# Performance work log

Measured on AMD Instinct MI355X. Metric: run time of the kernel, lower is better.

## Reference

```python
import jax, jax.numpy as jnp
import numpy as np


def grid_sample_bilinear(img, grid):
    """Replicates torch F.grid_sample(mode='bilinear', padding_mode='zeros',
    align_corners=False). img: [B,C,Hin,Win]; grid: [B,Ho,Wo,2] in [-1,1]
    with grid[...,0]=x (width), grid[...,1]=y (height). Returns [B,C,Ho,Wo]."""
    B, C, Hin, Win = img.shape
    x = (grid[..., 0] + 1.0) * (Win * 0.5) - 0.5  # unnormalized pixel coords
    y = (grid[..., 1] + 1.0) * (Hin * 0.5) - 0.5
    x0 = jnp.floor(x)
    y0 = jnp.floor(y)
    wx1 = x - x0
    wy1 = y - y0

    def tap(xi, yi, w):
        valid = ((xi >= 0) & (xi < Win) & (yi >= 0) & (yi < Hin)).astype(img.dtype)
        xc = jnp.clip(xi, 0, Win - 1).astype(jnp.int32)
        yc = jnp.clip(yi, 0, Hin - 1).astype(jnp.int32)
        def gather_one(im, yb, xb, wb):
            return im[:, yb, xb] * wb[None]  # [C,Ho,Wo]
        return jax.vmap(gather_one)(img, yc, xc, valid * w)

    return (tap(x0, y0, (1.0 - wx1) * (1.0 - wy1))
            + tap(x0 + 1.0, y0, wx1 * (1.0 - wy1))
            + tap(x0, y0 + 1.0, (1.0 - wx1) * wy1)
            + tap(x0 + 1.0, y0 + 1.0, wx1 * wy1))


def setup_inputs() -> dict:
    key = jax.random.key(0)
    k_uv, k1, k2, k3, k4 = jax.random.split(key, 5)
    W, H = 2048, 2048
    B, Ho, Wo = 8, 1024, 1024
    return {
        "uv": jax.random.uniform(k_uv, (B, Ho, Wo, 2), dtype=jnp.float32),
        "layer1": jax.random.normal(k1, (1, 1, W, H), dtype=jnp.float32),
        "layer2": jax.random.normal(k2, (1, 1, W // 2, H // 2), dtype=jnp.float32),
        "layer3": jax.random.normal(k3, (1, 1, W // 4, H // 4), dtype=jnp.float32),
        "layer4": jax.random.normal(k4, (1, 1, W // 8, H // 8), dtype=jnp.float32),
    }


def reference(uv, layer1, layer2, layer3, layer4):
    B = uv.shape[0]
    grid = uv * 2.0 - 1.0
    y = None
    for layer in (layer1, layer2, layer3, layer4):
        img = jnp.broadcast_to(layer, (B,) + layer.shape[1:])  # repeat(B,1,1,1)
        s = grid_sample_bilinear(img, grid)
        y = s if y is None else y + s
    return y  # [B,1,Ho,Wo]
```

## Files before the change

### kernel.cpp

```cpp
#include <hip/hip_runtime.h>
#include <hip/hip_fp16.h>


typedef unsigned int u32x2 __attribute__((ext_vector_type(2)));
typedef unsigned int u32x4 __attribute__((ext_vector_type(4)));
typedef float f32x4 __attribute__((ext_vector_type(4)));

#define K 1024
#define CHUNK 4096
#define HB 4096
#define SEG (CHUNK * 256)
#define NXCD 8

__device__ __forceinline__ int binof(float u, float v) {
    int bx = min(max((int)(u * 32.0f), 0), 31);
    int by = min(max((int)(v * 32.0f), 0), 31);
    return by * 32 + bx;
}

__global__ __launch_bounds__(256) void repack_hist_kernel(
    const float* __restrict__ l1, const float* __restrict__ l2,
    const float* __restrict__ l3, const float* __restrict__ l4,
    __half2* __restrict__ r1, __half2* __restrict__ r2,
    __half2* __restrict__ r3, __half2* __restrict__ r4,
    const float2* __restrict__ uv, unsigned* __restrict__ hist, int n) {
    const int n1 = 2048 * 2048, n2 = 1024 * 1024, n3 = 512 * 512, n4 = 256 * 256;
    int i = blockIdx.x * 256 + threadIdx.x;
    {
        const float* __restrict__ src = nullptr;
        __half2* __restrict__ dst = nullptr;
        int S = 0, logS = 0, j = 0;
        if (i < n1) {
            src = l1; dst = r1; S = 2048; logS = 11; j = i;
        } else if (i < n1 + n2) {
            src = l2; dst = r2; S = 1024; logS = 10; j = i - n1;
        } else if (i < n1 + n2 + n3) {
            src = l3; dst = r3; S = 512; logS = 9; j = i - (n1 + n2);
        } else if (i < n1 + n2 + n3 + n4) {
            src = l4; dst = r4; S = 256; logS = 8; j = i - (n1 + n2 + n3);
        }
        if (src) {
            int y = j >> logS;
            float a = src[j];
            float b = src[(y < S - 1) ? (j + S) : j];
            dst[j] = __halves2half2(__float2half(a), __float2half(b));
        }
    }
    if (hist == nullptr) return;
    int base = blockIdx.x * HB;
    if (base >= n) return;
    __shared__ unsigned cnt[K];
    for (int b = threadIdx.x; b < K; b += 256) cnt[b] = 0u;
    __syncthreads();
    int m = min(HB, n - base);
    const f32x4* uv4 = (const f32x4*)(uv + base);
    int npair = m >> 1;
    for (int k2 = threadIdx.x; k2 < npair; k2 += 256) {
        f32x4 q = __builtin_nontemporal_load(&uv4[k2]);
        atomicAdd(&cnt[binof(q.x, q.y)], 1u);
        atomicAdd(&cnt[binof(q.z, q.w)], 1u);
    }
    if ((m & 1) && threadIdx.x == 0) {
        float2 q = uv[base + m - 1];
        atomicAdd(&cnt[binof(q.x, q.y)], 1u);
    }
    __syncthreads();
    int seg = base / SEG;
    unsigned* gh = hist + (size_t)seg * K;
    for (int b = threadIdx.x; b < K; b += 256) {
        unsigned v = cnt[b];
        if (v) atomicAdd(&gh[b], v);
    }
}

__global__ __launch_bounds__(256) void scan_kernel(
    const unsigned* __restrict__ hist, unsigned* __restrict__ cursor) {
    int seg = blockIdx.x;
    const unsigned* h = hist + (size_t)seg * K;
    unsigned* c = cursor + (size_t)seg * K;
    __shared__ unsigned part[256];
    int t = threadIdx.x;
    unsigned v0 = h[t * 4], v1 = h[t * 4 + 1], v2 = h[t * 4 + 2], v3 = h[t * 4 + 3];
    unsigned s1 = v0, s2 = v0 + v1, s3 = v0 + v1 + v2;
    part[t] = s3 + v3;
    __syncthreads();
    for (int off = 1; off < 256; off <<= 1) {
        unsigned x = (t >= off) ? part[t - off] : 0u;
        __syncthreads();
        part[t] += x;
        __syncthreads();
    }
    unsigned tb = (t > 0) ? part[t - 1] : 0u;
    unsigned segstart = (unsigned)((size_t)seg * SEG);
    c[t * 4] = segstart + tb;
    c[t * 4 + 1] = segstart + tb + s1;
    c[t * 4 + 2] = segstart + tb + s2;
    c[t * 4 + 3] = segstart + tb + s3;
}

__global__ __launch_bounds__(256) void partition_kernel(
    const float2* __restrict__ uv, unsigned* __restrict__ cursor,
    float2* __restrict__ uv_s, unsigned* __restrict__ invp, int n, int pinned) {
    __shared__ float2 ssort[CHUNK];
    __shared__ unsigned cnt[K];
    __shared__ unsigned lbase[K];
    __shared__ unsigned gdiff[K];
    __shared__ unsigned part[256];
    int t = threadIdx.x;
    int blk = blockIdx.x;
    int c = pinned ? ((blk % NXCD) * (SEG / CHUNK) + blk / NXCD) : blk;
    int cb = c * CHUNK;
    if (cb >= n) return;
    int cnum = min(CHUNK, n - cb);
    int seg = cb / SEG;

    for (int b = t; b < K; b += 256) cnt[b] = 0u;
    __syncthreads();
    const f32x4* uv4 = (const f32x4*)(uv + cb);
    int npair = cnum >> 1;
    for (int k2 = t; k2 < npair; k2 += 256) {
        f32x4 q = uv4[k2];
        atomicAdd(&cnt[binof(q.x, q.y)], 1u);
        atomicAdd(&cnt[binof(q.z, q.w)], 1u);
    }
    if ((cnum & 1) && t == 0) {
        float2 q = uv[cb + cnum - 1];
        atomicAdd(&cnt[binof(q.x, q.y)], 1u);
    }
    __syncthreads();
    {
        unsigned v0 = cnt[t * 4], v1 = cnt[t * 4 + 1], v2 = cnt[t * 4 + 2],
                 v3 = cnt[t * 4 + 3];
        unsigned s1 = v0, s2 = v0 + v1, s3 = v0 + v1 + v2;
        part[t] = s3 + v3;
        __syncthreads();
        for (int off = 1; off < 256; off <<= 1) {
            unsigned x = (t >= off) ? part[t - off] : 0u;
            __syncthreads();
            part[t] += x;
            __syncthreads();
        }
        unsigned tb = (t > 0) ? part[t - 1] : 0u;
        unsigned lb[4] = {tb, tb + s1, tb + s2, tb + s3};
        unsigned cv[4] = {v0, v1, v2, v3};
        for (int j = 0; j < 4; ++j) {
            int b = t * 4 + j;
            lbase[b] = lb[j];
            unsigned goff =
                cv[j] ? atomicAdd(&cursor[(size_t)seg * K + b], cv[j]) : 0u;
            gdiff[b] = goff - lb[j];
        }
    }
    __syncthreads();
    for (int b = t; b < K; b += 256) cnt[b] = 0u;
    __syncthreads();
    for (int k2 = t; k2 < npair; k2 += 256) {
        f32x4 q = uv4[k2];
        int ba = binof(q.x, q.y);
        unsigned sa = lbase[ba] + atomicAdd(&cnt[ba], 1u);
        ssort[sa] = make_float2(q.x, q.y);
        int bb = binof(q.z, q.w);
        unsigned sb = lbase[bb] + atomicAdd(&cnt[bb], 1u);
        ssort[sb] = make_float2(q.z, q.w);
        if (invp) {
            u32x2 iv;
            iv.x = gdiff[ba] + sa;
            iv.y = gdiff[bb] + sb;
            *(u32x2*)(invp + cb + k2 * 2) = iv;
        }
    }
    if ((cnum & 1) && t == 0) {
        float2 q = uv[cb + cnum - 1];
        int b = binof(q.x, q.y);
        unsigned s = lbase[b] + atomicAdd(&cnt[b], 1u);
        ssort[s] = q;
        if (invp) invp[cb + cnum - 1] = gdiff[b] + s;
    }
    __syncthreads();
    for (int s = t; s < cnum; s += 256) {
        float2 q = ssort[s];
        int b = binof(q.x, q.y);
        uv_s[gdiff[b] + (unsigned)s] = q;
    }
}

__global__ __launch_bounds__(256) void partition_idx_kernel(
    const float2* __restrict__ uv, const unsigned* __restrict__ hist,
    unsigned* __restrict__ cursor, float2* __restrict__ uv_s,
    unsigned* __restrict__ idxp, int n, int pinned) {
    __shared__ float2 suv[CHUNK];
    __shared__ unsigned short slid[CHUNK];
    __shared__ unsigned cnt[K];
    __shared__ unsigned lbase[K];
    __shared__ unsigned goff[K];
    __shared__ unsigned part[256];
    int t = threadIdx.x;
    int blk = blockIdx.x;
    int c = pinned ? ((blk % NXCD) * (SEG / CHUNK) + blk / NXCD) : blk;
    int cb = c * CHUNK;
    if (cb >= n) return;
    int cnum = min(CHUNK, n - cb);
    int seg = cb / SEG;
    unsigned segstart = (unsigned)((size_t)seg * SEG);
    {
        const f32x4* uv4 = (const f32x4*)(uv + cb);
        int npair = cnum >> 1;
        for (int k2 = t; k2 < npair; k2 += 256) {
            f32x4 q = uv4[k2];
            suv[k2 * 2] = make_float2(q.x, q.y);
            suv[k2 * 2 + 1] = make_float2(q.z, q.w);
        }
        if ((cnum & 1) && t == 0) suv[cnum - 1] = uv[cb + cnum - 1];
    }
    for (int b = t; b < K; b += 256) cnt[b] = 0u;
    __syncthreads();
    for (int k = t; k < cnum; k += 256)
        atomicAdd(&cnt[binof(suv[k].x, suv[k].y)], 1u);
    __syncthreads();
    {
        unsigned v0 = cnt[t * 4], v1 = cnt[t * 4 + 1], v2 = cnt[t * 4 + 2],
                 v3 = cnt[t * 4 + 3];
        unsigned s1 = v0, s2 = v0 + v1, s3 = v0 + v1 + v2;
        part[t] = s3 + v3;
        __syncthreads();
        for (int off = 1; off < 256; off <<= 1) {
            unsigned x = (t >= off) ? part[t - off] : 0u;
            __syncthreads();
            part[t] += x;
            __syncthreads();
        }
        unsigned tb = (t > 0) ? part[t - 1] : 0u;
        lbase[t * 4] = tb;
        lbase[t * 4 + 1] = tb + s1;
        lbase[t * 4 + 2] = tb + s2;
        lbase[t * 4 + 3] = tb + s3;
    }
    __syncthreads();
    {
        const unsigned* h = hist + (size_t)seg * K;
        unsigned v0 = h[t * 4], v1 = h[t * 4 + 1], v2 = h[t * 4 + 2],
                 v3 = h[t * 4 + 3];
        unsigned s1 = v0, s2 = v0 + v1, s3 = v0 + v1 + v2;
        part[t] = s3 + v3;
        __syncthreads();
        for (int off = 1; off < 256; off <<= 1) {
            unsigned x = (t >= off) ? part[t - off] : 0u;
            __syncthreads();
            part[t] += x;
            __syncthreads();
        }
        unsigned tb = (t > 0) ? part[t - 1] : 0u;
        unsigned sbv[4] = {tb, tb + s1, tb + s2, tb + s3};
        for (int j = 0; j < 4; ++j) {
            int b = t * 4 + j;
            unsigned cc = cnt[b];
            unsigned r = cc ? atomicAdd(&cursor[(size_t)seg * K + b], cc) : 0u;
            goff[b] = segstart + sbv[j] + r;
        }
    }
    __syncthreads();
    for (int b = t; b < K; b += 256) cnt[b] = 0u;
    __syncthreads();
    for (int k = t; k < cnum; k += 256) {
        int b = binof(suv[k].x, suv[k].y);
        unsigned r = atomicAdd(&cnt[b], 1u);
        slid[lbase[b] + r] = (unsigned short)k;
    }
    __syncthreads();
    for (int s = t; s < cnum; s += 256) {
        int lid = slid[s];
        float2 q = suv[lid];
        int b = binof(q.x, q.y);
        unsigned pos = goff[b] + ((unsigned)s - lbase[b]);
        uv_s[pos] = q;
        idxp[pos] = (unsigned)(cb + lid);
    }
}

__device__ __forceinline__ float sample_level(const __half2* __restrict__ R,
                                              const int S, const float gx,
                                              const float gy) {
    const float halfS = 0.5f * (float)S;
    float x = (gx + 1.0f) * halfS - 0.5f;
    float y = (gy + 1.0f) * halfS - 0.5f;
    float xf = floorf(x), yf = floorf(y);
    float wx = x - xf, wy = y - yf;
    int x0 = (int)xf, y0 = (int)yf;

    int yc = min(max(y0, 0), S - 1);
    float wa = (y0 >= 0) ? (1.0f - wy) : wy;
    if (y0 < -1 || y0 >= S) wa = 0.0f;
    float wb = (y0 >= 0 && y0 < S - 1) ? wy : 0.0f;

    int xb = min(max(x0, 0), S - 2);
    bool xin = (x0 >= 0) && (x0 <= S - 2);
    float wxa = xin ? (1.0f - wx) : ((x0 == -1) ? wx : 0.0f);
    float wxb = xin ? wx : ((x0 == S - 1) ? (1.0f - wx) : 0.0f);

    uint2 q;
    __builtin_memcpy(&q, (const char*)(R + (size_t)yc * (size_t)S + xb), 8);
    __half2 ca = *(const __half2*)&q.x;
    __half2 cb = *(const __half2*)&q.y;
    float2 fa = __half22float2(ca);
    float2 fb = __half22float2(cb);
    float cola = fmaf(wa, fa.x, wb * fa.y);
    float colb = fmaf(wa, fb.x, wb * fb.y);
    return fmaf(wxa, cola, wxb * colb);
}

__device__ __forceinline__ float sample_point(const __half2* __restrict__ r1,
                                              const __half2* __restrict__ r2,
                                              const __half2* __restrict__ r3,
                                              const __half2* __restrict__ r4,
                                              float ux, float uy) {
    float gx = ux * 2.0f - 1.0f;
    float gy = uy * 2.0f - 1.0f;
    float acc = sample_level(r1, 2048, gx, gy);
    acc += sample_level(r2, 1024, gx, gy);
    acc += sample_level(r3, 512, gx, gy);
    acc += sample_level(r4, 256, gx, gy);
    return acc;
}

__global__ __launch_bounds__(256) void lappyr_sample4(
    const float2* __restrict__ uv_s, const __half2* __restrict__ r1,
    const __half2* __restrict__ r2, const __half2* __restrict__ r3,
    const __half2* __restrict__ r4, float* __restrict__ val_s, int n,
    int pinned) {
    int blk = blockIdx.x;
    int sb = pinned ? ((blk % NXCD) * (SEG / 1024) + blk / NXCD) : blk;
    int base = sb * 1024 + threadIdx.x * 4;
    if (base + 3 < n) {
        const f32x4* u4 = (const f32x4*)(uv_s + base);
        f32x4 a = __builtin_nontemporal_load(u4);
        f32x4 b = __builtin_nontemporal_load(u4 + 1);
        f32x4 res;
        res.x = sample_point(r1, r2, r3, r4, a.x, a.y);
        res.y = sample_point(r1, r2, r3, r4, a.z, a.w);
        res.z = sample_point(r1, r2, r3, r4, b.x, b.y);
        res.w = sample_point(r1, r2, r3, r4, b.z, b.w);
        *(f32x4*)(val_s + base) = res;
    } else {
        for (int j = 0; j < 4; ++j) {
            int p = base + j;
            if (p < n) {
                float2 q = uv_s[p];
                val_s[p] = sample_point(r1, r2, r3, r4, q.x, q.y);
            }
        }
    }
}

__global__ __launch_bounds__(256) void lappyr_unsort4(
    const unsigned* __restrict__ inv, const float* __restrict__ val_s,
    float* __restrict__ out, int n, int pinned) {
    int blk = blockIdx.x;
    int sb = pinned ? ((blk % NXCD) * (SEG / 1024) + blk / NXCD) : blk;
    int base = sb * 1024 + threadIdx.x * 4;
    if (base + 3 < n) {
        u32x4 iv = __builtin_nontemporal_load((const u32x4*)(inv + base));
        f32x4 res;
        res.x = val_s[iv.x];
        res.y = val_s[iv.y];
        res.z = val_s[iv.z];
        res.w = val_s[iv.w];
        __builtin_nontemporal_store(res, (f32x4*)(out + base));
    } else {
        for (int j = 0; j < 4; ++j) {
            int p = base + j;
            if (p < n) out[p] = val_s[inv[p]];
        }
    }
}

__global__ __launch_bounds__(256) void lappyr_sample_sorted(
    const float2* __restrict__ uv_s, const unsigned* __restrict__ idx_s,
    const __half2* __restrict__ r1, const __half2* __restrict__ r2,
    const __half2* __restrict__ r3, const __half2* __restrict__ r4,
    float* __restrict__ out, int n, int pinned) {
    int blk = blockIdx.x;
    int sb = pinned ? ((blk % NXCD) * (SEG / 512) + blk / NXCD) : blk;
    int i = sb * 256 + threadIdx.x;
    int p0 = i * 2;
    if (p0 >= n) return;
    if (p0 + 1 < n) {
        f32x4 q = __builtin_nontemporal_load((const f32x4*)uv_s + i);
        u32x2 id = __builtin_nontemporal_load((const u32x2*)idx_s + i);
        float a0 = sample_point(r1, r2, r3, r4, q.x, q.y);
        float a1 = sample_point(r1, r2, r3, r4, q.z, q.w);
        out[id.x] = a0;
        out[id.y] = a1;
    } else {
        float2 q = uv_s[p0];
        out[idx_s[p0]] = sample_point(r1, r2, r3, r4, q.x, q.y);
    }
}

__global__ __launch_bounds__(256) void lappyr_sample_kernel(
    const float2* __restrict__ uv, const __half2* __restrict__ r1,
    const __half2* __restrict__ r2, const __half2* __restrict__ r3,
    const __half2* __restrict__ r4, float* __restrict__ out, int n) {
    int i = blockIdx.x * blockDim.x + threadIdx.x;
    if (i >= n) return;
    float2 p = uv[i];
    out[i] = sample_point(r1, r2, r3, r4, p.x, p.y);
}

__device__ __forceinline__ float bilin_f32(const float* __restrict__ img,
                                           const int S, const float gx,
                                           const float gy) {
    const float halfS = 0.5f * (float)S;
    float x = (gx + 1.0f) * halfS - 0.5f;
    float y = (gy + 1.0f) * halfS - 0.5f;
    float xf = floorf(x), yf = floorf(y);
    float wx = x - xf, wy = y - yf;
    int x0 = (int)xf, y0 = (int)yf, x1 = x0 + 1, y1 = y0 + 1;
    float ex0 = (x0 >= 0 && x0 < S) ? (1.0f - wx) : 0.0f;
    float ex1 = (x1 >= 0 && x1 < S) ? wx : 0.0f;
    float ey0 = (y0 >= 0 && y0 < S) ? (1.0f - wy) : 0.0f;
    float ey1 = (y1 >= 0 && y1 < S) ? wy : 0.0f;
    int xc0 = min(max(x0, 0), S - 1), xc1 = min(max(x1, 0), S - 1);
    int yc0 = min(max(y0, 0), S - 1), yc1 = min(max(y1, 0), S - 1);
    const float* r0 = img + (size_t)yc0 * S;
    const float* r1 = img + (size_t)yc1 * S;
    return ey0 * fmaf(ex0, r0[xc0], ex1 * r0[xc1]) +
           ey1 * fmaf(ex0, r1[xc0], ex1 * r1[xc1]);
}

__global__ __launch_bounds__(256) void lappyr_f32_kernel(
    const float2* __restrict__ uv, const float* __restrict__ l1,
    const float* __restrict__ l2, const float* __restrict__ l3,
    const float* __restrict__ l4, float* __restrict__ out, int n) {
    int i = blockIdx.x * blockDim.x + threadIdx.x;
    if (i >= n) return;
    float2 p = uv[i];
    float gx = p.x * 2.0f - 1.0f;
    float gy = p.y * 2.0f - 1.0f;
    float acc = bilin_f32(l1, 2048, gx, gy);
    acc += bilin_f32(l2, 1024, gx, gy);
    acc += bilin_f32(l3, 512, gx, gy);
    acc += bilin_f32(l4, 256, gx, gy);
    out[i] = acc;
}

extern "C" void kernel_launch(void* const* d_in, const int* in_sizes, int n_in,
                              void* d_out, int out_size, void* d_ws, size_t ws_size,
                              hipStream_t stream) {
    const float2* uv = (const float2*)d_in[0];
    const float* l1 = (const float*)d_in[1];
    const float* l2 = (const float*)d_in[2];
    const float* l3 = (const float*)d_in[3];
    const float* l4 = (const float*)d_in[4];
    float* out = (float*)d_out;
    int n = out_size;

    const size_t n1 = 2048u * 2048u, n2 = 1024u * 1024u, n3 = 512u * 512u,
                 n4 = 256u * 256u;
    const size_t ntot = n1 + n2 + n3 + n4;
    const size_t rep_bytes = ntot * sizeof(__half2);

    int nseg = (n + SEG - 1) / SEG;
    size_t tbl_bytes = (size_t)nseg * K * 4 * 2;

    size_t off_uvs = (rep_bytes + 255) & ~(size_t)255;
    size_t off_inv = off_uvs + (size_t)n * 8;
    size_t off_val = off_inv + (size_t)n * 4;
    size_t off_hist2 = (off_val + (size_t)n * 4 + 255) & ~(size_t)255;
    size_t need2 = off_hist2 + tbl_bytes;
    size_t off_idx = off_uvs + (size_t)n * 8;
    size_t off_hist1 = (off_idx + (size_t)n * 4 + 255) & ~(size_t)255;
    size_t need1 = off_hist1 + tbl_bytes;

    int repack_blocks = (int)((ntot + 255) / 256);

    if (ws_size >= rep_bytes) {
        char* ws = (char*)d_ws;
        __half2* r1 = (__half2*)ws;
        __half2* r2 = r1 + n1;
        __half2* r3 = r2 + n2;
        __half2* r4 = r3 + n3;
        int pinned = (n == NXCD * SEG) ? 1 : 0;
        int hist_blocks = (n + HB - 1) / HB;
        int ga = max(repack_blocks, hist_blocks);
        int nchunks = (n + CHUNK - 1) / CHUNK;
        if (ws_size >= need2 && n > 0) {
            float2* uv_s = (float2*)(ws + off_uvs);
            unsigned* inv = (unsigned*)(ws + off_inv);
            float* val_s = (float*)(ws + off_val);
            unsigned* hist = (unsigned*)(ws + off_hist2);
            unsigned* cursor = hist + (size_t)nseg * K;
            hipMemsetAsync(hist, 0, (size_t)nseg * K * 4, stream);
            repack_hist_kernel<<<ga, 256, 0, stream>>>(l1, l2, l3, l4, r1, r2, r3,
                                                       r4, uv, hist, n);
            scan_kernel<<<nseg, 256, 0, stream>>>(hist, cursor);
            partition_kernel<<<nchunks, 256, 0, stream>>>(uv, cursor, uv_s, inv,
                                                          n, pinned);
            int nb4 = (n + 1023) / 1024;
            lappyr_sample4<<<nb4, 256, 0, stream>>>(uv_s, r1, r2, r3, r4, val_s,
                                                    n, pinned);
            lappyr_unsort4<<<nb4, 256, 0, stream>>>(inv, val_s, out, n, pinned);
        } else if (ws_size >= need1 && n > 0) {
            float2* uv_s = (float2*)(ws + off_uvs);
            unsigned* idx_s = (unsigned*)(ws + off_idx);
            unsigned* hist = (unsigned*)(ws + off_hist1);
            unsigned* cursor = hist + (size_t)nseg * K;
            hipMemsetAsync(hist, 0, tbl_bytes, stream);
            repack_hist_kernel<<<ga, 256, 0, stream>>>(l1, l2, l3, l4, r1, r2, r3,
                                                       r4, uv, hist, n);
            partition_idx_kernel<<<nchunks, 256, 0, stream>>>(
                uv, hist, cursor, uv_s, idx_s, n, pinned);
            int nh = (n + 1) / 2;
            lappyr_sample_sorted<<<(nh + 255) / 256, 256, 0, stream>>>(
                uv_s, idx_s, r1, r2, r3, r4, out, n, pinned);
        } else {
            repack_hist_kernel<<<repack_blocks, 256, 0, stream>>>(
                l1, l2, l3, l4, r1, r2, r3, r4, uv, nullptr, n);
            lappyr_sample_kernel<<<(n + 255) / 256, 256, 0, stream>>>(
                uv, r1, r2, r3, r4, out, n);
        }
    } else {
        lappyr_f32_kernel<<<(n + 255) / 256, 256, 0, stream>>>(uv, l1, l2, l3, l4,
                                                               out, n);
    }
}
```

Baseline: 312.3 us.

## Precompute per-chunk histograms and deterministic cursors; vectorize pyramid repack

```diff
diff --git a/kernel.cpp b/kernel.cpp
--- a/kernel.cpp
+++ b/kernel.cpp
@@ -18,36 +18,47 @@
     return by * 32 + bx;
 }
 
+__device__ __forceinline__ unsigned pack2(float lo, float hi) {
+    __half2 h = __halves2half2(__float2half(lo), __float2half(hi));
+    unsigned w;
+    __builtin_memcpy(&w, &h, 4);
+    return w;
+}
+
 __global__ __launch_bounds__(256) void repack_hist_kernel(
     const float* __restrict__ l1, const float* __restrict__ l2,
     const float* __restrict__ l3, const float* __restrict__ l4,
     __half2* __restrict__ r1, __half2* __restrict__ r2,
     __half2* __restrict__ r3, __half2* __restrict__ r4,
-    const float2* __restrict__ uv, unsigned* __restrict__ hist, int n) {
+    const float2* __restrict__ uv, unsigned* __restrict__ seghist,
+    unsigned* __restrict__ chist, int n) {
     const int n1 = 2048 * 2048, n2 = 1024 * 1024, n3 = 512 * 512, n4 = 256 * 256;
-    int i = blockIdx.x * 256 + threadIdx.x;
     {
+        int e = (blockIdx.x * 256 + threadIdx.x) * 4;
         const float* __restrict__ src = nullptr;
         __half2* __restrict__ dst = nullptr;
         int S = 0, logS = 0, j = 0;
-        if (i < n1) {
-            src = l1; dst = r1; S = 2048; logS = 11; j = i;
-        } else if (i < n1 + n2) {
-            src = l2; dst = r2; S = 1024; logS = 10; j = i - n1;
-        } else if (i < n1 + n2 + n3) {
-            src = l3; dst = r3; S = 512; logS = 9; j = i - (n1 + n2);
-        } else if (i < n1 + n2 + n3 + n4) {
-            src = l4; dst = r4; S = 256; logS = 8; j = i - (n1 + n2 + n3);
+        if (e < n1) {
+            src = l1; dst = r1; S = 2048; logS = 11; j = e;
+        } else if (e < n1 + n2) {
+            src = l2; dst = r2; S = 1024; logS = 10; j = e - n1;
+        } else if (e < n1 + n2 + n3) {
+            src = l3; dst = r3; S = 512; logS = 9; j = e - (n1 + n2);
+        } else if (e < n1 + n2 + n3 + n4) {
+            src = l4; dst = r4; S = 256; logS = 8; j = e - (n1 + n2 + n3);
         }
         if (src) {
             int y = j >> logS;
-            float a = src[j];
-            float b = src[(y < S - 1) ? (j + S) : j];
-            dst[j] = __halves2half2(__float2half(a), __float2half(b));
-        }
-    }
-    if (hist == nullptr) return;
-    int base = blockIdx.x * HB;
+            f32x4 a = *(const f32x4*)(src + j);
+            f32x4 b = *(const f32x4*)(src + ((y < S - 1) ? (j + S) : j));
+            u32x4 o = {pack2(a.x, b.x), pack2(a.y, b.y), pack2(a.z, b.z),
+                       pack2(a.w, b.w)};
+            *(u32x4*)(dst + j) = o;
+        }
+    }
+    if (seghist == nullptr) return;
+    int c = blockIdx.x;
+    int base = c * HB;
     if (base >= n) return;
     __shared__ unsigned cnt[K];
     for (int b = threadIdx.x; b < K; b += 256) cnt[b] = 0u;
@@ -66,19 +77,22 @@
     }
     __syncthreads();
     int seg = base / SEG;
-    unsigned* gh = hist + (size_t)seg * K;
+    unsigned* gh = seghist + (size_t)seg * K;
     for (int b = threadIdx.x; b < K; b += 256) {
         unsigned v = cnt[b];
+        if (chist) chist[(size_t)c * K + b] = v;
         if (v) atomicAdd(&gh[b], v);
     }
 }
 
-__global__ __launch_bounds__(256) void scan_kernel(
-    const unsigned* __restrict__ hist, unsigned* __restrict__ cursor) {
-    int seg = blockIdx.x;
-    const unsigned* h = hist + (size_t)seg * K;
-    unsigned* c = cursor + (size_t)seg * K;
+__global__ __launch_bounds__(256) void cursor_kernel(
+    const unsigned* __restrict__ seghist, const unsigned* __restrict__ chist,
+    unsigned* __restrict__ cursor, int nchunks) {
+    int seg = blockIdx.x >> 6;
+    int grp = blockIdx.x & 63;
+    const unsigned* h = seghist + (size_t)seg * K;
     __shared__ unsigned part[256];
+    __shared__ unsigned base[K];
     int t = threadIdx.x;
     unsigned v0 = h[t * 4], v1 = h[t * 4 + 1], v2 = h[t * 4 + 2], v3 = h[t * 4 + 3];
     unsigned s1 = v0, s2 = v0 + v1, s3 = v0 + v1 + v2;
@@ -91,16 +105,35 @@
         __syncthreads();
     }
     unsigned tb = (t > 0) ? part[t - 1] : 0u;
-    unsigned segstart = (unsigned)((size_t)seg * SEG);
-    c[t * 4] = segstart + tb;
-    c[t * 4 + 1] = segstart + tb + s1;
-    c[t * 4 + 2] = segstart + tb + s2;
-    c[t * 4 + 3] = segstart + tb + s3;
+    unsigned segstart = (unsigned)seg * (unsigned)SEG;
+    base[t * 4] = segstart + tb;
+    base[t * 4 + 1] = segstart + tb + s1;
+    base[t * 4 + 2] = segstart + tb + s2;
+    base[t * 4 + 3] = segstart + tb + s3;
+    __syncthreads();
+    int wave = t >> 6, lane = t & 63;
+    int c0 = seg * (SEG / CHUNK);
+    for (int j = wave; j < 16; j += 4) {
+        int b = grp * 16 + j;
+        unsigned run = 0;
+        for (int r = 0; r < 4; ++r) {
+            int c = r * 64 + lane;
+            unsigned v = (c0 + c < nchunks) ? chist[(size_t)(c0 + c) * K + b] : 0u;
+            unsigned x = v;
+            for (int d = 1; d < 64; d <<= 1) {
+                unsigned y = __shfl_up(x, d);
+                if (lane >= d) x += y;
+            }
+            cursor[((size_t)seg * K + b) * 256 + c] = base[b] + (x - v) + run;
+            run += __shfl(x, 63);
+        }
+    }
 }
 
 __global__ __launch_bounds__(256) void partition_kernel(
-    const float2* __restrict__ uv, unsigned* __restrict__ cursor,
-    float2* __restrict__ uv_s, unsigned* __restrict__ invp, int n, int pinned) {
+    const float2* __restrict__ uv, const unsigned* __restrict__ chist,
+    const unsigned* __restrict__ cursor, float2* __restrict__ uv_s,
+    unsigned* __restrict__ invp, int n, int pinned) {
     __shared__ float2 ssort[CHUNK];
     __shared__ unsigned cnt[K];
     __shared__ unsigned lbase[K];
@@ -112,27 +145,13 @@
     int cb = c * CHUNK;
     if (cb >= n) return;
     int cnum = min(CHUNK, n - cb);
-    int seg = cb / SEG;
-
-    for (int b = t; b < K; b += 256) cnt[b] = 0u;
-    __syncthreads();
-    const f32x4* uv4 = (const f32x4*)(uv + cb);
-    int npair = cnum >> 1;
-    for (int k2 = t; k2 < npair; k2 += 256) {
-        f32x4 q = uv4[k2];
-        atomicAdd(&cnt[binof(q.x, q.y)], 1u);
-        atomicAdd(&cnt[binof(q.z, q.w)], 1u);
-    }
-    if ((cnum & 1) && t == 0) {
-        float2 q = uv[cb + cnum - 1];
-        atomicAdd(&cnt[binof(q.x, q.y)], 1u);
-    }
-    __syncthreads();
+    int seg = c / (SEG / CHUNK);
+    int cidx = c % (SEG / CHUNK);
+
+    u32x4 hv = *(const u32x4*)(chist + (size_t)c * K + t * 4);
     {
-        unsigned v0 = cnt[t * 4], v1 = cnt[t * 4 + 1], v2 = cnt[t * 4 + 2],
-                 v3 = cnt[t * 4 + 3];
-        unsigned s1 = v0, s2 = v0 + v1, s3 = v0 + v1 + v2;
-        part[t] = s3 + v3;
+        unsigned s1 = hv.x, s2 = hv.x + hv.y, s3 = hv.x + hv.y + hv.z;
+        part[t] = s3 + hv.w;
         __syncthreads();
         for (int off = 1; off < 256; off <<= 1) {
             unsigned x = (t >= off) ? part[t - off] : 0u;
@@ -142,18 +161,16 @@
         }
         unsigned tb = (t > 0) ? part[t - 1] : 0u;
         unsigned lb[4] = {tb, tb + s1, tb + s2, tb + s3};
-        unsigned cv[4] = {v0, v1, v2, v3};
         for (int j = 0; j < 4; ++j) {
             int b = t * 4 + j;
             lbase[b] = lb[j];
-            unsigned goff =
-                cv[j] ? atomicAdd(&cursor[(size_t)seg * K + b], cv[j]) : 0u;
-            gdiff[b] = goff - lb[j];
-        }
-    }
-    __syncthreads();
-    for (int b = t; b < K; b += 256) cnt[b] = 0u;
-    __syncthreads();
+            gdiff[b] = cursor[((size_t)seg * K + b) * (SEG / CHUNK) + cidx] - lb[j];
+            cnt[b] = 0u;
+        }
+    }
+    __syncthreads();
+    const f32x4* uv4 = (const f32x4*)(uv + cb);
+    int npair = cnum >> 1;
     for (int k2 = t; k2 < npair; k2 += 256) {
         f32x4 q = uv4[k2];
         int ba = binof(q.x, q.y);
@@ -460,18 +477,24 @@
     const size_t rep_bytes = ntot * sizeof(__half2);
 
     int nseg = (n + SEG - 1) / SEG;
-    size_t tbl_bytes = (size_t)nseg * K * 4 * 2;
+    int nchunks = (n + CHUNK - 1) / CHUNK;
+    int cps = SEG / CHUNK;
+
+    size_t chist_b = (size_t)nseg * cps * K * 4;
+    size_t seg_b = (size_t)nseg * K * 4;
+    size_t tbl = chist_b + seg_b + chist_b;
+    size_t val_region = ((size_t)n * 4 > tbl) ? (size_t)n * 4 : tbl;
 
     size_t off_uvs = (rep_bytes + 255) & ~(size_t)255;
     size_t off_inv = off_uvs + (size_t)n * 8;
-    size_t off_val = off_inv + (size_t)n * 4;
-    size_t off_hist2 = (off_val + (size_t)n * 4 + 255) & ~(size_t)255;
-    size_t need2 = off_hist2 + tbl_bytes;
+    size_t off_val = (off_inv + (size_t)n * 4 + 255) & ~(size_t)255;
+    size_t need2 = off_val + val_region;
+    size_t tbl1 = (size_t)nseg * K * 4 * 2;
     size_t off_idx = off_uvs + (size_t)n * 8;
     size_t off_hist1 = (off_idx + (size_t)n * 4 + 255) & ~(size_t)255;
-    size_t need1 = off_hist1 + tbl_bytes;
-
-    int repack_blocks = (int)((ntot + 255) / 256);
+    size_t need1 = off_hist1 + tbl1;
+
+    int repack_blocks = (int)((ntot / 4 + 255) / 256);
 
     if (ws_size >= rep_bytes) {
         char* ws = (char*)d_ws;
@@ -482,19 +505,20 @@
         int pinned = (n == NXCD * SEG) ? 1 : 0;
         int hist_blocks = (n + HB - 1) / HB;
         int ga = max(repack_blocks, hist_blocks);
-        int nchunks = (n + CHUNK - 1) / CHUNK;
         if (ws_size >= need2 && n > 0) {
             float2* uv_s = (float2*)(ws + off_uvs);
             unsigned* inv = (unsigned*)(ws + off_inv);
             float* val_s = (float*)(ws + off_val);
-            unsigned* hist = (unsigned*)(ws + off_hist2);
-            unsigned* cursor = hist + (size_t)nseg * K;
-            hipMemsetAsync(hist, 0, (size_t)nseg * K * 4, stream);
+            unsigned* chist = (unsigned*)(ws + off_val);
+            unsigned* seghist = (unsigned*)(ws + off_val + chist_b);
+            unsigned* cursor = (unsigned*)(ws + off_val + chist_b + seg_b);
+            (void)hipMemsetAsync(chist, 0, chist_b + seg_b, stream);
             repack_hist_kernel<<<ga, 256, 0, stream>>>(l1, l2, l3, l4, r1, r2, r3,
-                                                       r4, uv, hist, n);
-            scan_kernel<<<nseg, 256, 0, stream>>>(hist, cursor);
-            partition_kernel<<<nchunks, 256, 0, stream>>>(uv, cursor, uv_s, inv,
-                                                          n, pinned);
+                                                       r4, uv, seghist, chist, n);
+            cursor_kernel<<<nseg * 64, 256, 0, stream>>>(seghist, chist, cursor,
+                                                         nchunks);
+            partition_kernel<<<nchunks, 256, 0, stream>>>(uv, chist, cursor, uv_s,
+                                                          inv, n, pinned);
             int nb4 = (n + 1023) / 1024;
             lappyr_sample4<<<nb4, 256, 0, stream>>>(uv_s, r1, r2, r3, r4, val_s,
                                                     n, pinned);
@@ -504,9 +528,9 @@
             unsigned* idx_s = (unsigned*)(ws + off_idx);
             unsigned* hist = (unsigned*)(ws + off_hist1);
             unsigned* cursor = hist + (size_t)nseg * K;
-            hipMemsetAsync(hist, 0, tbl_bytes, stream);
+            (void)hipMemsetAsync(hist, 0, tbl1, stream);
             repack_hist_kernel<<<ga, 256, 0, stream>>>(l1, l2, l3, l4, r1, r2, r3,
-                                                       r4, uv, hist, n);
+                                                       r4, uv, hist, nullptr, n);
             partition_idx_kernel<<<nchunks, 256, 0, stream>>>(
                 uv, hist, cursor, uv_s, idx_s, n, pinned);
             int nh = (n + 1) / 2;
@@ -514,7 +538,7 @@
                 uv_s, idx_s, r1, r2, r3, r4, out, n, pinned);
         } else {
             repack_hist_kernel<<<repack_blocks, 256, 0, stream>>>(
-                l1, l2, l3, l4, r1, r2, r3, r4, uv, nullptr, n);
+                l1, l2, l3, l4, r1, r2, r3, r4, uv, nullptr, nullptr, n);
             lappyr_sample_kernel<<<(n + 255) / 256, 256, 0, stream>>>(
                 uv, r1, r2, r3, r4, out, n);
         }
```

New measurement: 302.6 us. 3.1% less time.
